# Kernel optimization log

Hardware: AMD Instinct MI355X
Metric: run time of the kernel (lower is better)

The kernel has to match this reference:

```python
import jax, jax.numpy as jnp
import numpy as np

KP_EXTENT = 1.2  # influence radius of each kernel point (init arg KP_extent)
SHADOW_COORD = 1e6  # shadow point coordinate for padding (as in original KPConv)


def setup_inputs() -> dict:
    key = jax.random.key(0)
    k1, k2, k3, k4, k5, k6 = jax.random.split(key, 6)
    N, Ns, H, K, Cin, Cout = 20000, 20000, 40, 15, 128, 128
    q_pts = jax.random.uniform(k1, (N, 3), dtype=jnp.float32)
    s_pts = jax.random.uniform(k2, (Ns, 3), dtype=jnp.float32)
    neighb_inds = jax.random.randint(k3, (N, H), 0, Ns, dtype=jnp.int32)
    x = jax.random.normal(k4, (Ns, Cin), dtype=jnp.float32)
    # kernel point positions inside the sphere (stand-in for load_kernels output)
    kernel_points = jax.random.normal(k5, (K, 3), dtype=jnp.float32) * 0.5
    kernel_points = kernel_points.at[0].set(0.0)  # fixed='center'
    weights = jax.random.normal(k6, (K, Cin, Cout), dtype=jnp.float32) * (1.0 / np.sqrt(Cin))
    return {"q_pts": q_pts, "s_pts": s_pts, "neighb_inds": neighb_inds,
            "x": x, "kernel_points": kernel_points, "weights": weights}


def reference(q_pts, s_pts, neighb_inds, x, kernel_points, weights):
    # Pad support points with a far-away shadow point and features with a zero row,
    # so out-of-range neighbor index Ns contributes nothing (original KPConv trick).
    s_pad = jnp.concatenate([s_pts, jnp.full((1, s_pts.shape[1]), SHADOW_COORD, s_pts.dtype)], axis=0)
    x_pad = jnp.concatenate([x, jnp.zeros((1, x.shape[1]), x.dtype)], axis=0)

    # Gather neighbor coords, center on query points: [N, H, 3]
    neighbors = s_pad[neighb_inds] - q_pts[:, None, :]

    # Squared distance to every kernel point: [N, H, K]
    diff = neighbors[:, :, None, :] - kernel_points[None, None, :, :]
    sq_dist = jnp.sum(diff * diff, axis=-1)

    # Linear influence weights, aggregation_mode='sum': [N, K, H]
    all_weights = jnp.clip(1.0 - jnp.sqrt(sq_dist) / KP_EXTENT, 0.0, None)
    all_weights = jnp.swapaxes(all_weights, 1, 2)

    # Gather neighbor features: [N, H, Cin]
    neighb_x = x_pad[neighb_inds]

    # Influence-weighted aggregation over neighbors: [N, K, Cin]
    weighted = jnp.einsum('nkh,nhc->nkc', all_weights, neighb_x)

    # Per-kernel-point linear maps, summed over kernel points: [N, Cout]
    out = jnp.einsum('nkc,kcd->nd', weighted, weights)
    return out
```

## Files before the change

### kernel.cpp

```cpp
#include <hip/hip_runtime.h>

#define KP   15
#define HN   40
#define CIN  128
#define COUT 128
#define KDIM (KP*CIN)
#define KP_EXT_INV (1.0f/1.2f)

typedef __bf16 bf16x8 __attribute__((ext_vector_type(8)));
typedef float  f32x4  __attribute__((ext_vector_type(4)));

__device__ inline void async_copy16(const void* g, void* lds) {
    __builtin_amdgcn_global_load_lds(
        (const __attribute__((address_space(1))) unsigned int*)g,
        (__attribute__((address_space(3))) unsigned int*)lds, 16, 0, 0);
}

__global__ __launch_bounds__(256)
void kpconv_prep(const float* __restrict__ x, const float* __restrict__ W,
                 __bf16* __restrict__ xb, __bf16* __restrict__ Wt,
                 int nx_elems, int nxB)
{
    __shared__ float sW[32][133];
    const int b = blockIdx.x;
    const int t = threadIdx.x;

    if (b < nxB) {
        const int e0 = (b*256 + t) * 8;
        if (e0 + 8 <= nx_elems) {
            const float4 f0 = *(const float4*)(x + e0);
            const float4 f1 = *(const float4*)(x + e0 + 4);
            bf16x8 v;
            v[0]=(__bf16)f0.x; v[1]=(__bf16)f0.y; v[2]=(__bf16)f0.z; v[3]=(__bf16)f0.w;
            v[4]=(__bf16)f1.x; v[5]=(__bf16)f1.y; v[6]=(__bf16)f1.z; v[7]=(__bf16)f1.w;
            *(bf16x8*)(xb + e0) = v;
        } else {
            for (int e = e0; e < nx_elems; ++e) xb[e] = (__bf16)x[e];
        }
    } else {
        const int kc0 = (b - nxB) * 32;
        #pragma unroll
        for (int i = 0; i < 4; ++i) {
            const int off = t*4 + i*1024;
            const int r = off >> 7, c = off & 127;
            const float4 f = *(const float4*)(W + (size_t)(kc0 + r)*COUT + c);
            sW[r][c+0]=f.x; sW[r][c+1]=f.y; sW[r][c+2]=f.z; sW[r][c+3]=f.w;
        }
        __syncthreads();
        #pragma unroll
        for (int i = 0; i < 2; ++i) {
            const int id = t + i*256;
            const int d  = id >> 2, ch = id & 3;
            bf16x8 v;
            #pragma unroll
            for (int j = 0; j < 8; ++j) v[j] = (__bf16)sW[ch*8 + j][d];
            *(bf16x8*)(Wt + (size_t)d*KDIM + kc0 + ch*8) = v;
        }
    }
}

__global__ __launch_bounds__(256, 4)
void kpconv_aggregate(const float* __restrict__ q_pts,
                      const float* __restrict__ s_pts,
                      const int*   __restrict__ nb,
                      const __bf16* __restrict__ xb,
                      const float* __restrict__ kpts,
                      __bf16* __restrict__ wsA,
                      int N, int Ns)
{
    __shared__ __align__(16) __bf16 sXt[4][4][128][8];
    __shared__ __align__(16) float4 s_nd[4][HN];
    __shared__ int                  s_idx[4][HN];

    const int t  = threadIdx.x;
    const int wv = t >> 6;
    const int l  = t & 63;
    const int n  = blockIdx.x * 4 + wv;

    if (l < HN) {
        int idx = nb[n*HN + l];
        float dx, dy, dz;
        if (idx >= 0 && idx < Ns) {
            dx = s_pts[idx*3+0] - q_pts[n*3+0];
            dy = s_pts[idx*3+1] - q_pts[n*3+1];
            dz = s_pts[idx*3+2] - q_pts[n*3+2];
        } else { idx = 0; dx = dy = dz = 2.0e6f; }
        s_idx[wv][l] = idx;
        s_nd[wv][l]  = make_float4(dx, dy, dz, 0.f);
    }
    __syncthreads();

    const int m = l & 15;
    const int q = l >> 4;
    float kx = 0.f, ky = 0.f, kz = 0.f;
    if (m < KP) { kx = kpts[m*3+0]; ky = kpts[m*3+1]; kz = kpts[m*3+2]; }

    bf16x8 wfrag[2];
    #pragma unroll
    for (int ks = 0; ks < 2; ++ks) {
        #pragma unroll
        for (int j = 0; j < 8; ++j) {
            const int h = ks*32 + q*8 + j;
            float w = 0.f;
            if (m < KP && h < HN) {
                float4 nd = s_nd[wv][h];
                float dx = nd.x - kx, dy = nd.y - ky, dz = nd.z - kz;
                w = fmaxf(1.0f - sqrtf(dx*dx + dy*dy + dz*dz) * KP_EXT_INV, 0.f);
            }
            wfrag[ks][j] = (__bf16)w;
        }
    }

    f32x4 acc[8];
    #pragma unroll
    for (int nt = 0; nt < 8; ++nt) acc[nt] = (f32x4){0.f, 0.f, 0.f, 0.f};

    const int c8 = l & 15;

    for (int ks = 0; ks < 2; ++ks) {
        const int hpBeg = ks ? 16 : 0;
        const int hpEnd = ks ? 20 : 16;
        for (int hp = hpBeg + (l >> 4); hp < hpEnd; hp += 4) {
            const int h0 = 2*hp;
            const uint4 a = *(const uint4*)(xb + (size_t)s_idx[wv][h0  ]*CIN + c8*8);
            const uint4 bb= *(const uint4*)(xb + (size_t)s_idx[wv][h0+1]*CIN + c8*8);
            const unsigned int av[4] = {a.x, a.y, a.z, a.w};
            const unsigned int bv[4] = {bb.x, bb.y, bb.z, bb.w};
            const int hl = h0 - ks*32;
            const int hc = hl >> 3;
            const int dw = hp & 3;
            unsigned int* plane = (unsigned int*)&sXt[wv][hc][0][0];
            #pragma unroll
            for (int j = 0; j < 8; ++j) {
                const unsigned int lo = (av[j>>1] >> ((j&1)*16)) & 0xFFFFu;
                const unsigned int hi = (bv[j>>1] >> ((j&1)*16)) & 0xFFFFu;
                const int p = c8*8 + (j ^ (c8 & 7));
                plane[p*4 + dw] = lo | (hi << 16);
            }
        }
        __syncthreads();

        #pragma unroll
        for (int nt = 0; nt < 8; ++nt) {
            const int cc = nt*16 + m;
            const int p  = (cc & ~7) | ((cc & 7) ^ ((cc >> 3) & 7));
            bf16x8 bfrag = *(const bf16x8*)&sXt[wv][q][p][0];
            acc[nt] = __builtin_amdgcn_mfma_f32_16x16x32_bf16(
                          wfrag[ks], bfrag, acc[nt], 0, 0, 0);
        }
        __syncthreads();
    }

    #pragma unroll
    for (int nt = 0; nt < 8; ++nt) {
        #pragma unroll
        for (int r = 0; r < 4; ++r) {
            const int row = q*4 + r;
            if (row < KP)
                wsA[(size_t)n*KDIM + row*CIN + nt*16 + m] = (__bf16)acc[nt][r];
        }
    }
}

#define BM 32
#define BK 128

__global__ __launch_bounds__(256, 2)
void kpconv_gemm(const __bf16* __restrict__ A,
                 const __bf16* __restrict__ Bt,
                 float* __restrict__ out, int M)
{
    __shared__ __align__(16) __bf16 sA[BM*BK];
    __shared__ __align__(16) __bf16 sB[COUT*BK];

    const int t     = threadIdx.x;
    const int wv    = t >> 6;
    const int l     = t & 63;
    const int mlane = l & 15;
    const int q     = l >> 4;
    const int m0    = blockIdx.x * BM;

    const int rA = t >> 4;
    const int pA = t & 15;

    f32x4 acc[2][2];
    #pragma unroll
    for (int i = 0; i < 2; ++i)
        #pragma unroll
        for (int j = 0; j < 2; ++j) acc[i][j] = (f32x4){0.f,0.f,0.f,0.f};

    for (int k0 = 0; k0 < KDIM; k0 += BK) {
        #pragma unroll
        for (int pass = 0; pass < 2; ++pass) {
            const int r  = rA + pass*16;
            const int ch = pA ^ (r & 15);
            async_copy16(A + (size_t)(m0 + r)*KDIM + k0 + ch*8,
                         (char*)sA + pass*4096 + wv*1024 + l*16);
        }
        #pragma unroll
        for (int pass = 0; pass < 8; ++pass) {
            const int r  = rA + pass*16;
            const int ch = pA ^ (r & 15);
            async_copy16(Bt + (size_t)r*KDIM + k0 + ch*8,
                         (char*)sB + pass*4096 + wv*1024 + l*16);
        }
        __syncthreads();

        #pragma unroll
        for (int ksi = 0; ksi < 4; ++ksi) {
            bf16x8 af[2], bfr[2];
            #pragma unroll
            for (int mt = 0; mt < 2; ++mt) {
                const int row = mt*16 + mlane;
                const int p   = (ksi*4 + q) ^ (row & 15);
                af[mt] = *(const bf16x8*)&sA[row*BK + p*8];
            }
            #pragma unroll
            for (int j = 0; j < 2; ++j) {
                const int row = (wv*2 + j)*16 + mlane;
                const int p   = (ksi*4 + q) ^ (row & 15);
                bfr[j] = *(const bf16x8*)&sB[row*BK + p*8];
            }
            #pragma unroll
            for (int mt = 0; mt < 2; ++mt)
                #pragma unroll
                for (int j = 0; j < 2; ++j)
                    acc[mt][j] = __builtin_amdgcn_mfma_f32_16x16x32_bf16(
                                     af[mt], bfr[j], acc[mt][j], 0, 0, 0);
        }
        __syncthreads();
    }

    #pragma unroll
    for (int mt = 0; mt < 2; ++mt)
        #pragma unroll
        for (int j = 0; j < 2; ++j)
            #pragma unroll
            for (int r = 0; r < 4; ++r)
                out[(size_t)(m0 + mt*16 + q*4 + r)*COUT + (wv*2+j)*16 + mlane]
                    = acc[mt][j][r];
}

#define TM 8
#define WSTR (KP*CIN + 4)

__global__ __launch_bounds__(256, 2)
void kpconv_fused(const float* __restrict__ q_pts,
                  const float* __restrict__ s_pts,
                  const int*   __restrict__ nb,
                  const float* __restrict__ x,
                  const float* __restrict__ kpts,
                  const float* __restrict__ W,
                  float* __restrict__ out,
                  int N, int Ns)
{
    __shared__ float s_kp[KP*3];
    __shared__ float s_nd2[HN*3];
    __shared__ int   s_idx2[HN];
    __shared__ float s_w[KP][HN];
    __shared__ float s_wt[TM*WSTR];

    const int t  = threadIdx.x;
    const int n0 = (int)blockIdx.x * TM;
    if (t < KP*3) s_kp[t] = kpts[t];
    const int c = t & (CIN-1);
    const int g = t >> 7;

    for (int m = 0; m < TM; ++m) {
        const int n = n0 + m;
        if (t < HN) {
            float dx = 1e6f, dy = 1e6f, dz = 1e6f;
            int idx = 0;
            if (n < N) {
                idx = nb[n*HN + t];
                if (idx >= 0 && idx < Ns) {
                    dx = s_pts[idx*3+0] - q_pts[n*3+0];
                    dy = s_pts[idx*3+1] - q_pts[n*3+1];
                    dz = s_pts[idx*3+2] - q_pts[n*3+2];
                } else idx = 0;
            }
            s_idx2[t] = idx;
            s_nd2[t*3+0] = dx; s_nd2[t*3+1] = dy; s_nd2[t*3+2] = dz;
        }
        __syncthreads();
        for (int task = t; task < KP*HN; task += 256) {
            const int k = task / HN;
            const int h = task - k*HN;
            const float dx = s_nd2[h*3+0] - s_kp[k*3+0];
            const float dy = s_nd2[h*3+1] - s_kp[k*3+1];
            const float dz = s_nd2[h*3+2] - s_kp[k*3+2];
            s_w[k][h] = fmaxf(1.0f - sqrtf(dx*dx+dy*dy+dz*dz)*KP_EXT_INV, 0.0f);
        }
        __syncthreads();
        float facc[8];
        #pragma unroll
        for (int j = 0; j < 8; ++j) facc[j] = 0.0f;
        #pragma unroll 8
        for (int h = 0; h < HN; ++h) {
            const float xv = x[s_idx2[h]*CIN + c];
            #pragma unroll
            for (int j = 0; j < 8; ++j) {
                const int k = g + 2*j;
                if (k < KP) facc[j] += s_w[k][h] * xv;
            }
        }
        #pragma unroll
        for (int j = 0; j < 8; ++j) {
            const int k = g + 2*j;
            if (k < KP) s_wt[m*WSTR + k*CIN + c] = facc[j];
        }
        __syncthreads();
    }

    const int m3 = t >> 5;
    const int d0 = (t & 31) * 4;
    const float* wm = &s_wt[m3*WSTR];
    float ax = 0.f, ay = 0.f, az = 0.f, aw = 0.f;
    #pragma unroll 4
    for (int kc = 0; kc < KP*CIN; ++kc) {
        const float  wvv = wm[kc];
        const float4 wr = *(const float4*)&W[kc*COUT + d0];
        ax += wvv * wr.x; ay += wvv * wr.y; az += wvv * wr.z; aw += wvv * wr.w;
    }
    const int n = n0 + m3;
    if (n < N) {
        float4 o; o.x = ax; o.y = ay; o.z = az; o.w = aw;
        *(float4*)&out[n*COUT + d0] = o;
    }
}

extern "C" void kernel_launch(void* const* d_in, const int* in_sizes, int n_in,
                              void* d_out, int out_size, void* d_ws, size_t ws_size,
                              hipStream_t stream) {
    const float* q_pts = (const float*)d_in[0];
    const float* s_pts = (const float*)d_in[1];
    const int*   nb    = (const int*)  d_in[2];
    const float* x     = (const float*)d_in[3];
    const float* kpts  = (const float*)d_in[4];
    const float* W     = (const float*)d_in[5];
    float* out = (float*)d_out;

    const int N  = in_sizes[0] / 3;
    const int Ns = in_sizes[1] / 3;
    const int nx = in_sizes[3];

    const size_t needA = (size_t)N * KDIM * sizeof(__bf16);
    const size_t needB = (size_t)COUT * KDIM * sizeof(__bf16);
    const size_t needX = (size_t)nx * sizeof(__bf16);

    if (ws_size >= needA + needB + needX && (N % 4) == 0 && (N % BM) == 0
        && (KDIM % 32) == 0) {
        __bf16* wsA = (__bf16*)d_ws;
        __bf16* wsB = (__bf16*)((char*)d_ws + needA);
        __bf16* wsX = (__bf16*)((char*)d_ws + needA + needB);

        const int nxB = (nx/8 + 255) / 256;
        const int nwB = KDIM / 32;
        hipLaunchKernelGGL(kpconv_prep, dim3(nxB + nwB), dim3(256), 0, stream,
                           x, W, wsX, wsB, nx, nxB);
        hipLaunchKernelGGL(kpconv_aggregate, dim3(N/4), dim3(256), 0, stream,
                           q_pts, s_pts, nb, wsX, kpts, wsA, N, Ns);
        hipLaunchKernelGGL(kpconv_gemm, dim3(N/BM), dim3(256), 0, stream,
                           wsA, wsB, out, N);
    } else {
        const int grid = (N + TM - 1) / TM;
        hipLaunchKernelGGL(kpconv_fused, dim3(grid), dim3(256), 0, stream,
                           q_pts, s_pts, nb, x, kpts, W, out, N, Ns);
    }
}
```

Baseline: 146.1 us.

## Replace block barriers with wave waits, swap MFMA operands, enlarge GEMM tile

The aggregate kernel now uses per-wave s_waitcnt instead of __syncthreads, since each wave only touches its own LDS slice. It packs bf16 pairs with v_perm and swaps the MFMA operand order so each lane can write four contiguous bf16 outputs as one vector store. The GEMM tile grows from 32 to 64 rows, with a higher occupancy hint and a bounds-clamped tail, so the B tile is reused across more A rows. The cost is more registers per GEMM thread and a reliance on wave-local LDS ordering without block barriers, which could be fragile.

Result: no change. 148.2 us (+1.4%).

```diff
diff --git a/kernel.cpp b/kernel.cpp
--- a/kernel.cpp
+++ b/kernel.cpp
@@ -8,6 +8,7 @@
 #define KP_EXT_INV (1.0f/1.2f)
 
 typedef __bf16 bf16x8 __attribute__((ext_vector_type(8)));
+typedef __bf16 bf16x4 __attribute__((ext_vector_type(4)));
 typedef float  f32x4  __attribute__((ext_vector_type(4)));
 
 __device__ inline void async_copy16(const void* g, void* lds) {
@@ -75,6 +76,8 @@
     const int t  = threadIdx.x;
     const int wv = t >> 6;
     const int l  = t & 63;
+    const int m  = l & 15;
+    const int q  = l >> 4;
     const int n  = blockIdx.x * 4 + wv;
 
     if (l < HN) {
@@ -88,10 +91,8 @@
         s_idx[wv][l] = idx;
         s_nd[wv][l]  = make_float4(dx, dy, dz, 0.f);
     }
-    __syncthreads();
-
-    const int m = l & 15;
-    const int q = l >> 4;
+    __asm__ __volatile__("s_waitcnt lgkmcnt(0)" ::: "memory");
+
     float kx = 0.f, ky = 0.f, kz = 0.f;
     if (m < KP) { kx = kpts[m*3+0]; ky = kpts[m*3+1]; kz = kpts[m*3+2]; }
 
@@ -105,7 +106,7 @@
             if (m < KP && h < HN) {
                 float4 nd = s_nd[wv][h];
                 float dx = nd.x - kx, dy = nd.y - ky, dz = nd.z - kz;
-                w = fmaxf(1.0f - sqrtf(dx*dx + dy*dy + dz*dz) * KP_EXT_INV, 0.f);
+                w = fmaxf(1.0f - sqrtf(dx*dx + dy*dy + dz*dz)*KP_EXT_INV, 0.f);
             }
             wfrag[ks][j] = (__bf16)w;
         }
@@ -113,59 +114,58 @@
 
     f32x4 acc[8];
     #pragma unroll
-    for (int nt = 0; nt < 8; ++nt) acc[nt] = (f32x4){0.f, 0.f, 0.f, 0.f};
-
-    const int c8 = l & 15;
-
+    for (int nt = 0; nt < 8; ++nt) acc[nt] = (f32x4){0.f,0.f,0.f,0.f};
+
+    #pragma unroll
     for (int ks = 0; ks < 2; ++ks) {
-        const int hpBeg = ks ? 16 : 0;
-        const int hpEnd = ks ? 20 : 16;
-        for (int hp = hpBeg + (l >> 4); hp < hpEnd; hp += 4) {
+        const int iters = ks ? 1 : 4;
+        #pragma unroll
+        for (int it = 0; it < iters; ++it) {
+            const int hp = ks*16 + it*4 + q;
             const int h0 = 2*hp;
-            const uint4 a = *(const uint4*)(xb + (size_t)s_idx[wv][h0  ]*CIN + c8*8);
-            const uint4 bb= *(const uint4*)(xb + (size_t)s_idx[wv][h0+1]*CIN + c8*8);
-            const unsigned int av[4] = {a.x, a.y, a.z, a.w};
-            const unsigned int bv[4] = {bb.x, bb.y, bb.z, bb.w};
+            const uint4 a  = *(const uint4*)(xb + (size_t)s_idx[wv][h0  ]*CIN + m*8);
+            const uint4 bb = *(const uint4*)(xb + (size_t)s_idx[wv][h0+1]*CIN + m*8);
+            const unsigned av[4] = {a.x, a.y, a.z, a.w};
+            const unsigned bv[4] = {bb.x, bb.y, bb.z, bb.w};
             const int hl = h0 - ks*32;
             const int hc = hl >> 3;
             const int dw = hp & 3;
-            unsigned int* plane = (unsigned int*)&sXt[wv][hc][0][0];
+            unsigned* plane = (unsigned*)&sXt[wv][hc][0][0];
             #pragma unroll
             for (int j = 0; j < 8; ++j) {
-                const unsigned int lo = (av[j>>1] >> ((j&1)*16)) & 0xFFFFu;
-                const unsigned int hi = (bv[j>>1] >> ((j&1)*16)) & 0xFFFFu;
-                const int p = c8*8 + (j ^ (c8 & 7));
-                plane[p*4 + dw] = lo | (hi << 16);
-            }
-        }
-        __syncthreads();
+                const unsigned v = __builtin_amdgcn_perm(
+                    bv[j>>1], av[j>>1], (j&1) ? 0x07060302u : 0x05040100u);
+                const int p = m*8 + (j ^ (m & 7));
+                plane[p*4 + dw] = v;
+            }
+        }
+        __asm__ __volatile__("s_waitcnt lgkmcnt(0)" ::: "memory");
 
         #pragma unroll
         for (int nt = 0; nt < 8; ++nt) {
             const int cc = nt*16 + m;
             const int p  = (cc & ~7) | ((cc & 7) ^ ((cc >> 3) & 7));
-            bf16x8 bfrag = *(const bf16x8*)&sXt[wv][q][p][0];
+            bf16x8 xf = *(const bf16x8*)&sXt[wv][q][p][0];
             acc[nt] = __builtin_amdgcn_mfma_f32_16x16x32_bf16(
-                          wfrag[ks], bfrag, acc[nt], 0, 0, 0);
-        }
-        __syncthreads();
-    }
-
-    #pragma unroll
-    for (int nt = 0; nt < 8; ++nt) {
-        #pragma unroll
-        for (int r = 0; r < 4; ++r) {
-            const int row = q*4 + r;
-            if (row < KP)
-                wsA[(size_t)n*KDIM + row*CIN + nt*16 + m] = (__bf16)acc[nt][r];
-        }
-    }
-}
-
-#define BM 32
+                          xf, wfrag[ks], acc[nt], 0, 0, 0);
+        }
+    }
+
+    if (m < KP) {
+        #pragma unroll
+        for (int nt = 0; nt < 8; ++nt) {
+            bf16x4 v;
+            #pragma unroll
+            for (int r = 0; r < 4; ++r) v[r] = (__bf16)acc[nt][r];
+            *(bf16x4*)(wsA + (size_t)n*KDIM + m*CIN + nt*16 + q*4) = v;
+        }
+    }
+}
+
+#define BM 64
 #define BK 128
 
-__global__ __launch_bounds__(256, 2)
+__global__ __launch_bounds__(256, 3)
 void kpconv_gemm(const __bf16* __restrict__ A,
                  const __bf16* __restrict__ Bt,
                  float* __restrict__ out, int M)
@@ -183,18 +183,19 @@
     const int rA = t >> 4;
     const int pA = t & 15;
 
-    f32x4 acc[2][2];
-    #pragma unroll
-    for (int i = 0; i < 2; ++i)
+    f32x4 acc[4][2];
+    #pragma unroll
+    for (int i = 0; i < 4; ++i)
         #pragma unroll
         for (int j = 0; j < 2; ++j) acc[i][j] = (f32x4){0.f,0.f,0.f,0.f};
 
     for (int k0 = 0; k0 < KDIM; k0 += BK) {
         #pragma unroll
-        for (int pass = 0; pass < 2; ++pass) {
+        for (int pass = 0; pass < 4; ++pass) {
             const int r  = rA + pass*16;
+            int rg = m0 + r; if (rg >= M) rg = M - 1;
             const int ch = pA ^ (r & 15);
-            async_copy16(A + (size_t)(m0 + r)*KDIM + k0 + ch*8,
+            async_copy16(A + (size_t)rg*KDIM + k0 + ch*8,
                          (char*)sA + pass*4096 + wv*1024 + l*16);
         }
         #pragma unroll
@@ -208,9 +209,9 @@
 
         #pragma unroll
         for (int ksi = 0; ksi < 4; ++ksi) {
-            bf16x8 af[2], bfr[2];
-            #pragma unroll
-            for (int mt = 0; mt < 2; ++mt) {
+            bf16x8 af[4], bfr[2];
+            #pragma unroll
+            for (int mt = 0; mt < 4; ++mt) {
                 const int row = mt*16 + mlane;
                 const int p   = (ksi*4 + q) ^ (row & 15);
                 af[mt] = *(const bf16x8*)&sA[row*BK + p*8];
@@ -222,7 +223,7 @@
                 bfr[j] = *(const bf16x8*)&sB[row*BK + p*8];
             }
             #pragma unroll
-            for (int mt = 0; mt < 2; ++mt)
+            for (int mt = 0; mt < 4; ++mt)
                 #pragma unroll
                 for (int j = 0; j < 2; ++j)
                     acc[mt][j] = __builtin_amdgcn_mfma_f32_16x16x32_bf16(
@@ -232,13 +233,15 @@
     }
 
     #pragma unroll
-    for (int mt = 0; mt < 2; ++mt)
+    for (int mt = 0; mt < 4; ++mt)
         #pragma unroll
         for (int j = 0; j < 2; ++j)
             #pragma unroll
-            for (int r = 0; r < 4; ++r)
-                out[(size_t)(m0 + mt*16 + q*4 + r)*COUT + (wv*2+j)*16 + mlane]
-                    = acc[mt][j][r];
+            for (int r = 0; r < 4; ++r) {
+                const int row = m0 + mt*16 + q*4 + r;
+                if (row < M)
+                    out[(size_t)row*COUT + (wv*2+j)*16 + mlane] = acc[mt][j][r];
+            }
 }
 
 #define TM 8
@@ -266,8 +269,8 @@
     const int c = t & (CIN-1);
     const int g = t >> 7;
 
-    for (int m = 0; m < TM; ++m) {
-        const int n = n0 + m;
+    for (int mm = 0; mm < TM; ++mm) {
+        const int n = n0 + mm;
         if (t < HN) {
             float dx = 1e6f, dy = 1e6f, dz = 1e6f;
             int idx = 0;
@@ -307,7 +310,7 @@
         #pragma unroll
         for (int j = 0; j < 8; ++j) {
             const int k = g + 2*j;
-            if (k < KP) s_wt[m*WSTR + k*CIN + c] = facc[j];
+            if (k < KP) s_wt[mm*WSTR + k*CIN + c] = facc[j];
         }
         __syncthreads();
     }
@@ -348,8 +351,7 @@
     const size_t needB = (size_t)COUT * KDIM * sizeof(__bf16);
     const size_t needX = (size_t)nx * sizeof(__bf16);
 
-    if (ws_size >= needA + needB + needX && (N % 4) == 0 && (N % BM) == 0
-        && (KDIM % 32) == 0) {
+    if (ws_size >= needA + needB + needX && (N % 4) == 0 && (KDIM % 128) == 0) {
         __bf16* wsA = (__bf16*)d_ws;
         __bf16* wsB = (__bf16*)((char*)d_ws + needA);
         __bf16* wsX = (__bf16*)((char*)d_ws + needA + needB);
@@ -360,7 +362,7 @@
                            x, W, wsX, wsB, nx, nxB);
         hipLaunchKernelGGL(kpconv_aggregate, dim3(N/4), dim3(256), 0, stream,
                            q_pts, s_pts, nb, wsX, kpts, wsA, N, Ns);
-        hipLaunchKernelGGL(kpconv_gemm, dim3(N/BM), dim3(256), 0, stream,
+        hipLaunchKernelGGL(kpconv_gemm, dim3((N + BM - 1)/BM), dim3(256), 0, stream,
                            wsA, wsB, out, N);
     } else {
         const int grid = (N + TM - 1) / TM;
```
